# Kernel optimization log

Hardware: AMD Instinct MI355X
Metric: run time of the kernel (lower is better)

Reference implementation:

```python
import jax, jax.numpy as jnp
import numpy as np
from jax import lax

N_WAY, N_SUPPORT, N_QUERY = 16, 256, 512
D_IN, D_EMB = 4096, 1024
N_CLUSTERS, MAX_ITER = 5, 100


def setup_inputs() -> dict:
    key = jax.random.key(0)
    k1, k2, kw, kb = jax.random.split(key, 4)
    support = jax.random.normal(k1, (N_WAY, N_SUPPORT, D_IN), jnp.float32)
    query = jax.random.normal(k2, (N_WAY, N_QUERY, D_IN), jnp.float32)
    W = jax.random.normal(kw, (D_IN, D_EMB), jnp.float32) / np.float32(np.sqrt(D_IN))
    b = jax.random.normal(kb, (D_EMB,), jnp.float32) * 0.01
    return {"support": support, "query": query, "W": W, "b": b}


def _sqdist(x, c):
    # x [n,d], c [k,d] -> [n,k] squared euclidean distances
    return (jnp.sum(x * x, -1, keepdims=True)
            - 2.0 * (x @ c.T)
            + jnp.sum(c * c, -1))


def _kmeans(x, init):
    # x [n,d], init [k,d]; fixed-iteration Lloyd's kmeans (converged state is a
    # fixed point of the update, matching the torch early-break semantics).
    n = x.shape[0]
    ones = jnp.ones((n,), x.dtype)

    def step(c, _):
        assign = jnp.argmin(_sqdist(x, c), axis=1)              # [n]
        sums = jax.ops.segment_sum(x, assign, num_segments=N_CLUSTERS)
        cnt = jax.ops.segment_sum(ones, assign, num_segments=N_CLUSTERS)
        # empty cluster keeps its old centroid
        new_c = jnp.where(cnt[:, None] > 0,
                          sums / jnp.maximum(cnt, 1.0)[:, None], c)
        return new_c, None

    c, _ = lax.scan(step, init, None, length=MAX_ITER)
    return c


def _forward(support, query, W, b):
    # encoder: shared linear over flattened (n_way * n) rows
    s = (support.reshape(-1, D_IN) @ W + b).reshape(N_WAY, N_SUPPORT, D_EMB)
    q = (query.reshape(-1, D_IN) @ W + b).reshape(N_WAY, N_QUERY, D_EMB)

    # per-class kmeans init: random subset of that class's support embeddings
    keys = jax.random.split(jax.random.key(42), N_WAY)

    def init_fn(key, class_emb):
        idx = jax.random.permutation(key, N_SUPPORT)[:N_CLUSTERS]
        return class_emb[idx]

    inits = jax.vmap(init_fn)(keys, s)                 # [n_way, k, d]
    cluster_protos = jax.vmap(_kmeans)(s, inits)       # [n_way, k, d]
    class_protos = cluster_protos.mean(axis=1)         # [n_way, d]

    # cdist(query_emb [b,n,d], protos [c,d]) -> [b,n,c]
    d2 = (jnp.sum(q * q, -1)[..., None]
          - 2.0 * jnp.einsum('bnd,cd->bnc', q, class_protos)
          + jnp.sum(class_protos * class_protos, -1))
    distances = jnp.sqrt(jnp.maximum(d2, 0.0))
    return -distances                                  # logits [n_way, n_query, n_classes]


def reference(support, query, W, b):
    return _forward(support, query, W, b)
```

## Files before the change

kernel.cpp:

```cpp
#include <hip/hip_runtime.h>
#include <cstdint>
#include <cstddef>


typedef __attribute__((ext_vector_type(4))) float f32x4;
typedef __attribute__((ext_vector_type(8))) short s16x8;
typedef __attribute__((ext_vector_type(4))) short s16x4;
typedef __attribute__((ext_vector_type(8))) __bf16 bf16x8;

__device__ __forceinline__ unsigned short f2bf(float f) {
  unsigned u = __float_as_uint(f);
  return (unsigned short)((u + 0x7FFFu + ((u >> 16) & 1u)) >> 16);
}
__device__ __forceinline__ float bf2f(unsigned short h) {
  return __uint_as_float(((unsigned)h) << 16);
}

typedef const __attribute__((address_space(1))) void GV;
typedef __attribute__((address_space(3))) void LV;
__device__ __forceinline__ void gload_lds16(const void* g, void* l) {
  __builtin_amdgcn_global_load_lds((GV*)g, (LV*)l, 16, 0, 0);
}
__device__ __forceinline__ f32x4 mfma16(bf16x8 a, bf16x8 b, f32x4 c) {
  return __builtin_amdgcn_mfma_f32_16x16x32_bf16(a, b, c, 0, 0, 0);
}
__device__ __forceinline__ float wave_sum(float v) {
#pragma unroll
  for (int st = 1; st < 64; st <<= 1) v += __shfl_xor(v, st);
  return v;
}

__device__ __forceinline__ void tf2x32(unsigned k0, unsigned k1, unsigned x0,
                                       unsigned x1, unsigned& y0, unsigned& y1) {
  unsigned ks0 = k0, ks1 = k1, ks2 = k0 ^ k1 ^ 0x1BD11BDAu;
  x0 += ks0; x1 += ks1;
  const int rA[4] = {13, 15, 26, 6};
  const int rB[4] = {17, 29, 16, 24};
#define ROTL(v, d) (((v) << (d)) | ((v) >> (32 - (d))))
#define RG(R)                                     \
  _Pragma("unroll") for (int i = 0; i < 4; i++) { \
    x0 += x1; x1 = ROTL(x1, R[i]); x1 ^= x0;      \
  }
  RG(rA); x0 += ks1; x1 += ks2 + 1u;
  RG(rB); x0 += ks2; x1 += ks0 + 2u;
  RG(rA); x0 += ks0; x1 += ks1 + 3u;
  RG(rB); x0 += ks1; x1 += ks2 + 4u;
  RG(rA); x0 += ks2; x1 += ks0 + 5u;
#undef RG
#undef ROTL
  y0 = x0; y1 = x1;
}

__global__ __launch_bounds__(256) void prep_k(
    const float* __restrict__ W, const float* __restrict__ sup,
    const float* __restrict__ qry, short* __restrict__ WhiT,
    short* __restrict__ WloT, short* __restrict__ Shi,
    short* __restrict__ Slo, short* __restrict__ Qhi) {
  __shared__ float tile[64][65];
  int t = threadIdx.x;
  if (blockIdx.x < 1024) {
    int bk = blockIdx.x & 63, bn = blockIdx.x >> 6;
#pragma unroll
    for (int i = 0; i < 4; i++) {
      int row = i * 16 + (t >> 4);
      int col = (t & 15) * 4;
      f32x4 v =
          *(const f32x4*)(W + (size_t)(bk * 64 + row) * 1024 + bn * 64 + col);
      tile[row][col + 0] = v[0]; tile[row][col + 1] = v[1];
      tile[row][col + 2] = v[2]; tile[row][col + 3] = v[3];
    }
    __syncthreads();
#pragma unroll
    for (int i = 0; i < 4; i++) {
      int nrow = i * 16 + (t >> 4);
      int kcol = (t & 15) * 4;
      s16x4 hv, lv;
#pragma unroll
      for (int e = 0; e < 4; e++) {
        float v = tile[kcol + e][nrow];
        unsigned short h = f2bf(v);
        hv[e] = (short)h;
        lv[e] = (short)f2bf(v - bf2f(h));
      }
      size_t off = (size_t)(bn * 64 + nrow) * 4096 + bk * 64 + kcol;
      *(s16x4*)(WhiT + off) = hv;
      *(s16x4*)(WloT + off) = lv;
    }
  } else {
    const size_t sup_n8 = (size_t)4096 * 4096 / 8;
    const size_t tot_n8 = sup_n8 + (size_t)8192 * 4096 / 8;
    size_t stride = (size_t)(gridDim.x - 1024) * 256;
    for (size_t gid = (size_t)(blockIdx.x - 1024) * 256 + t; gid < tot_n8;
         gid += stride) {
      if (gid < sup_n8) {
        const float* src = sup + gid * 8;
        f32x4 v0 = *(const f32x4*)src, v1 = *(const f32x4*)(src + 4);
        s16x8 h, l;
#pragma unroll
        for (int e = 0; e < 4; e++) {
          unsigned short hh = f2bf(v0[e]);
          h[e] = (short)hh; l[e] = (short)f2bf(v0[e] - bf2f(hh));
        }
#pragma unroll
        for (int e = 0; e < 4; e++) {
          unsigned short hh = f2bf(v1[e]);
          h[4 + e] = (short)hh; l[4 + e] = (short)f2bf(v1[e] - bf2f(hh));
        }
        *(s16x8*)(Shi + gid * 8) = h;
        *(s16x8*)(Slo + gid * 8) = l;
      } else {
        size_t q = gid - sup_n8;
        const float* src = qry + q * 8;
        f32x4 v0 = *(const f32x4*)src, v1 = *(const f32x4*)(src + 4);
        s16x8 h;
#pragma unroll
        for (int e = 0; e < 4; e++) h[e] = (short)f2bf(v0[e]);
#pragma unroll
        for (int e = 0; e < 4; e++) h[4 + e] = (short)f2bf(v1[e]);
        *(s16x8*)(Qhi + q * 8) = h;
      }
    }
  }
}

__global__ __launch_bounds__(256) void gemm_sup_k(
    const short* __restrict__ Shi, const short* __restrict__ Slo,
    const short* __restrict__ WhiT, const short* __restrict__ WloT,
    const float* __restrict__ bias, float* __restrict__ emb) {
  __shared__ short lds[24576];
  short* Ah = lds;
  short* Al = lds + 4096;
  short* Bh = lds + 8192;
  short* Bl = lds + 16384;
  const int bid = blockIdx.x;
  const int bm = bid & 63, bn = bid >> 6;
  const int t = threadIdx.x, lane = t & 63, w = t >> 6;
  const int wr = w >> 1, wc = w & 1;
  const int fr = lane & 15, kg = lane >> 4;
  const int ls = lane >> 3, lc = lane & 7;
  const short* Ag = Shi + (size_t)bm * 64 * 4096;
  const short* Alg = Slo + (size_t)bm * 64 * 4096;
  f32x4 acc[2][4] = {};

  for (int kt = 0; kt < 64; ++kt) {
    const int k0 = kt * 64;
    __syncthreads();
    const int cch = (lc ^ ls) * 8;
#pragma unroll
    for (int j = 0; j < 2; j++) {
      int rowl = w * 16 + j * 8 + ls;
      size_t aoff = (size_t)rowl * 4096 + k0 + cch;
      int ldst = (w * 16 + j * 8) * 64;
      gload_lds16(Ag + aoff, Ah + ldst);
      gload_lds16(Alg + aoff, Al + ldst);
    }
#pragma unroll
    for (int j = 0; j < 4; j++) {
      int rowl = w * 32 + j * 8 + ls;
      size_t boff = (size_t)(bn * 128 + rowl) * 4096 + k0 + cch;
      int ldst = (w * 32 + j * 8) * 64;
      gload_lds16(WhiT + boff, Bh + ldst);
      gload_lds16(WloT + boff, Bl + ldst);
    }
    __syncthreads();
#pragma unroll
    for (int ks = 0; ks < 2; ++ks) {
      const int cx = ((ks * 4 + kg) ^ (fr & 7)) * 8;
      bf16x8 ahf[2], alf[2], bhf[4], blf[4];
#pragma unroll
      for (int mi = 0; mi < 2; mi++) {
        int arow = wr * 32 + mi * 16 + fr;
        ahf[mi] = __builtin_bit_cast(bf16x8, *(const s16x8*)(Ah + arow * 64 + cx));
        alf[mi] = __builtin_bit_cast(bf16x8, *(const s16x8*)(Al + arow * 64 + cx));
      }
#pragma unroll
      for (int ni = 0; ni < 4; ni++) {
        int brow = wc * 64 + ni * 16 + fr;
        bhf[ni] = __builtin_bit_cast(bf16x8, *(const s16x8*)(Bh + brow * 64 + cx));
        blf[ni] = __builtin_bit_cast(bf16x8, *(const s16x8*)(Bl + brow * 64 + cx));
      }
#pragma unroll
      for (int mi = 0; mi < 2; mi++)
#pragma unroll
        for (int ni = 0; ni < 4; ni++) {
          acc[mi][ni] = mfma16(ahf[mi], bhf[ni], acc[mi][ni]);
          acc[mi][ni] = mfma16(ahf[mi], blf[ni], acc[mi][ni]);
          acc[mi][ni] = mfma16(alf[mi], bhf[ni], acc[mi][ni]);
        }
    }
  }
#pragma unroll
  for (int ni = 0; ni < 4; ni++) {
    int gc = bn * 128 + wc * 64 + ni * 16 + fr;
    float bv = bias[gc];
#pragma unroll
    for (int mi = 0; mi < 2; mi++) {
      int gr = bm * 64 + wr * 32 + mi * 16 + kg * 4;
#pragma unroll
      for (int r = 0; r < 4; r++)
        emb[(size_t)(gr + r) * 1024 + gc] = acc[mi][ni][r] + bv;
    }
  }
}

__global__ __launch_bounds__(256) void gemm_qry_k(
    const short* __restrict__ Qhi, const short* __restrict__ WhiT,
    const float* __restrict__ bias, float* __restrict__ emb) {
  __shared__ short lds[16384];
  short* Ah = lds;
  short* Bh = lds + 8192;
  const int bid = blockIdx.x;
  const int bm = bid & 63, bn = bid >> 6;
  const int t = threadIdx.x, lane = t & 63, w = t >> 6;
  const int wr = w >> 1, wc = w & 1;
  const int fr = lane & 15, kg = lane >> 4;
  const int ls = lane >> 3, lc = lane & 7;
  const short* Ag = Qhi + (size_t)bm * 128 * 4096;
  f32x4 acc[4][4] = {};

  for (int kt = 0; kt < 64; ++kt) {
    const int k0 = kt * 64;
    __syncthreads();
    const int cch = (lc ^ ls) * 8;
#pragma unroll
    for (int j = 0; j < 4; j++) {
      int rowl = w * 32 + j * 8 + ls;
      size_t aoff = (size_t)rowl * 4096 + k0 + cch;
      size_t boff = (size_t)(bn * 128 + rowl) * 4096 + k0 + cch;
      int ldst = (w * 32 + j * 8) * 64;
      gload_lds16(Ag + aoff, Ah + ldst);
      gload_lds16(WhiT + boff, Bh + ldst);
    }
    __syncthreads();
#pragma unroll
    for (int ks = 0; ks < 2; ++ks) {
      const int cx = ((ks * 4 + kg) ^ (fr & 7)) * 8;
      bf16x8 ahf[4], bhf[4];
#pragma unroll
      for (int mi = 0; mi < 4; mi++) {
        int arow = wr * 64 + mi * 16 + fr;
        ahf[mi] = __builtin_bit_cast(bf16x8, *(const s16x8*)(Ah + arow * 64 + cx));
      }
#pragma unroll
      for (int ni = 0; ni < 4; ni++) {
        int brow = wc * 64 + ni * 16 + fr;
        bhf[ni] = __builtin_bit_cast(bf16x8, *(const s16x8*)(Bh + brow * 64 + cx));
      }
#pragma unroll
      for (int mi = 0; mi < 4; mi++)
#pragma unroll
        for (int ni = 0; ni < 4; ni++)
          acc[mi][ni] = mfma16(ahf[mi], bhf[ni], acc[mi][ni]);
    }
  }
#pragma unroll
  for (int ni = 0; ni < 4; ni++) {
    int gc = bn * 128 + wc * 64 + ni * 16 + fr;
    float bv = bias[gc];
#pragma unroll
    for (int mi = 0; mi < 4; mi++) {
      int gr = 4096 + bm * 128 + wr * 64 + mi * 16 + kg * 4;
#pragma unroll
      for (int r = 0; r < 4; r++)
        emb[(size_t)(gr + r) * 1024 + gc] = acc[mi][ni][r] + bv;
    }
  }
}

__global__ __launch_bounds__(256) void gemm_all_k(
    const float* __restrict__ sup, const float* __restrict__ qry,
    const short* __restrict__ WhiT, const short* __restrict__ WloT,
    const float* __restrict__ bias, float* __restrict__ emb) {
  __shared__ short lds[4 * 128 * 64];
  short* Ah = lds;
  short* Al = lds + 8192;
  short* Bh = lds + 16384;
  short* Bl = lds + 24576;
  const int bid = blockIdx.x;
  const int bm = bid % 96, bn = bid / 96;
  const bool is_sup = bm < 32;
  const int t = threadIdx.x, lane = t & 63, w = t >> 6;
  const int wr = w >> 1, wc = w & 1;
  const int fr = lane & 15, kg = lane >> 4;
  const float* Abase = is_sup ? (sup + (size_t)bm * 128 * 4096)
                              : (qry + (size_t)(bm - 32) * 128 * 4096);
  f32x4 acc[4][4] = {};
  const int ls = lane >> 3, lc = lane & 7;

  for (int kt = 0; kt < 64; ++kt) {
    const int k0 = kt * 64;
    __syncthreads();
#pragma unroll
    for (int i = 0; i < 4; i++) {
      int row = i * 32 + w * 8 + ls;
      const float* src = Abase + (size_t)row * 4096 + k0 + lc * 8;
      f32x4 v0 = *(const f32x4*)src;
      f32x4 v1 = *(const f32x4*)(src + 4);
      s16x8 hs;
#pragma unroll
      for (int e = 0; e < 4; e++) hs[e] = (short)f2bf(v0[e]);
#pragma unroll
      for (int e = 0; e < 4; e++) hs[4 + e] = (short)f2bf(v1[e]);
      int chunk = lc ^ (row & 7);
      *(s16x8*)(Ah + row * 64 + chunk * 8) = hs;
      if (is_sup) {
        s16x8 lsv;
#pragma unroll
        for (int e = 0; e < 4; e++)
          lsv[e] = (short)f2bf(v0[e] - bf2f((unsigned short)hs[e]));
#pragma unroll
        for (int e = 0; e < 4; e++)
          lsv[4 + e] = (short)f2bf(v1[e] - bf2f((unsigned short)hs[4 + e]));
        *(s16x8*)(Al + row * 64 + chunk * 8) = lsv;
      }
    }
#pragma unroll
    for (int j = 0; j < 4; j++) {
      int rowl = w * 32 + j * 8 + ls;
      int cch = (lc ^ (ls & 7)) * 8;
      size_t goff = (size_t)(bn * 128 + rowl) * 4096 + k0 + cch;
      gload_lds16(WhiT + goff, Bh + (w * 32 + j * 8) * 64);
      if (is_sup) gload_lds16(WloT + goff, Bl + (w * 32 + j * 8) * 64);
    }
    __syncthreads();
#pragma unroll
    for (int ks = 0; ks < 2; ++ks) {
      const int cx = ((ks * 4 + kg) ^ (fr & 7)) * 8;
      bf16x8 ahf[4], bhf[4];
#pragma unroll
      for (int mi = 0; mi < 4; mi++) {
        int arow = wr * 64 + mi * 16 + fr;
        ahf[mi] = __builtin_bit_cast(bf16x8, *(const s16x8*)(Ah + arow * 64 + cx));
      }
#pragma unroll
      for (int ni = 0; ni < 4; ni++) {
        int brow = wc * 64 + ni * 16 + fr;
        bhf[ni] = __builtin_bit_cast(bf16x8, *(const s16x8*)(Bh + brow * 64 + cx));
      }
      if (is_sup) {
        bf16x8 alf[4], blf[4];
#pragma unroll
        for (int mi = 0; mi < 4; mi++) {
          int arow = wr * 64 + mi * 16 + fr;
          alf[mi] =
              __builtin_bit_cast(bf16x8, *(const s16x8*)(Al + arow * 64 + cx));
        }
#pragma unroll
        for (int ni = 0; ni < 4; ni++) {
          int brow = wc * 64 + ni * 16 + fr;
          blf[ni] =
              __builtin_bit_cast(bf16x8, *(const s16x8*)(Bl + brow * 64 + cx));
        }
#pragma unroll
        for (int mi = 0; mi < 4; mi++)
#pragma unroll
          for (int ni = 0; ni < 4; ni++) {
            acc[mi][ni] = mfma16(ahf[mi], bhf[ni], acc[mi][ni]);
            acc[mi][ni] = mfma16(ahf[mi], blf[ni], acc[mi][ni]);
            acc[mi][ni] = mfma16(alf[mi], bhf[ni], acc[mi][ni]);
          }
      } else {
#pragma unroll
        for (int mi = 0; mi < 4; mi++)
#pragma unroll
          for (int ni = 0; ni < 4; ni++)
            acc[mi][ni] = mfma16(ahf[mi], bhf[ni], acc[mi][ni]);
      }
    }
  }
#pragma unroll
  for (int ni = 0; ni < 4; ni++) {
    int gc = bn * 128 + wc * 64 + ni * 16 + fr;
    float bv = bias[gc];
#pragma unroll
    for (int mi = 0; mi < 4; mi++) {
      int gr = bm * 128 + wr * 64 + mi * 16 + kg * 4;
#pragma unroll
      for (int r = 0; r < 4; r++)
        emb[(size_t)(gr + r) * 1024 + gc] = acc[mi][ni][r] + bv;
    }
  }
}

__global__ __launch_bounds__(256) void gramdiag_k(const float* __restrict__ emb,
                                                  float* __restrict__ G) {
  if (blockIdx.x < 256) {
    int c = blockIdx.x >> 4, tl = blockIdx.x & 15, ti = tl >> 2, tj = tl & 3;
    __shared__ float As[64][36];
    __shared__ float Bs[32][68];
    int t = threadIdx.x, ty = t >> 4, tx = t & 15;
    const float* base = emb + (size_t)c * 256 * 1024;
    float acc[4][4] = {};
    for (int k0 = 0; k0 < 1024; k0 += 32) {
      __syncthreads();
      {
        int r = t >> 2, seg = t & 3;
        const float* pa = base + (size_t)(ti * 64 + r) * 1024 + k0 + seg * 8;
        f32x4 va0 = *(const f32x4*)pa, va1 = *(const f32x4*)(pa + 4);
        *(f32x4*)(&As[r][seg * 8]) = va0;
        *(f32x4*)(&As[r][seg * 8 + 4]) = va1;
        const float* pb = base + (size_t)(tj * 64 + r) * 1024 + k0 + seg * 8;
        f32x4 vb0 = *(const f32x4*)pb, vb1 = *(const f32x4*)(pb + 4);
#pragma unroll
        for (int e = 0; e < 4; e++) Bs[seg * 8 + e][r] = vb0[e];
#pragma unroll
        for (int e = 0; e < 4; e++) Bs[seg * 8 + 4 + e][r] = vb1[e];
      }
      __syncthreads();
#pragma unroll 4
      for (int kk = 0; kk < 32; kk++) {
        float a0 = As[ty * 4 + 0][kk], a1 = As[ty * 4 + 1][kk];
        float a2 = As[ty * 4 + 2][kk], a3 = As[ty * 4 + 3][kk];
        f32x4 bv = *(const f32x4*)(&Bs[kk][tx * 4]);
#pragma unroll
        for (int jdx = 0; jdx < 4; jdx++) {
          acc[0][jdx] = fmaf(a0, bv[jdx], acc[0][jdx]);
          acc[1][jdx] = fmaf(a1, bv[jdx], acc[1][jdx]);
          acc[2][jdx] = fmaf(a2, bv[jdx], acc[2][jdx]);
          acc[3][jdx] = fmaf(a3, bv[jdx], acc[3][jdx]);
        }
      }
    }
#pragma unroll
    for (int i = 0; i < 4; i++) {
      int gr = ti * 64 + ty * 4 + i;
#pragma unroll
      for (int j = 0; j < 4; j++) {
        int gcl = tj * 64 + tx * 4 + j;
        if (gr != gcl)
          G[(size_t)c * 65536 + (size_t)gr * 256 + gcl] = acc[i][j];
      }
    }
  } else {
    int r = (blockIdx.x - 256) * 4 + (threadIdx.x >> 6);
    int lane = threadIdx.x & 63;
    const float* x = emb + (size_t)r * 1024;
    double acc = 0.0;
#pragma unroll
    for (int ch = 0; ch < 16; ch++) {
      float v = x[ch * 64 + lane];
      acc = fma((double)v, (double)v, acc);
    }
#pragma unroll
    for (int st = 1; st < 64; st <<= 1) acc += __shfl_xor(acc, st);
    if (lane == 0) {
      int c = r >> 8, i = r & 255;
      G[(size_t)c * 65536 + (size_t)i * 256 + i] = (float)acc;
    }
  }
}

#define APPLY1(db, nb, gg, p)                        \
  if ((db) & 1u)  s[p][0] += ((nb) & 1u)  ? (gg) : -(gg); \
  if ((db) & 2u)  s[p][1] += ((nb) & 2u)  ? (gg) : -(gg); \
  if ((db) & 4u)  s[p][2] += ((nb) & 4u)  ? (gg) : -(gg); \
  if ((db) & 8u)  s[p][3] += ((nb) & 8u)  ? (gg) : -(gg); \
  if ((db) & 16u) s[p][4] += ((nb) & 16u) ? (gg) : -(gg);

__global__ __launch_bounds__(64) void kmeans3_k(const float* __restrict__ G,
                                                float* __restrict__ wts) {
  const int c = blockIdx.x;
  const int lane = threadIdx.x;
  unsigned o0, o1, s0k, s1k;
  tf2x32(0u, 42u, 0u, (unsigned)c, o0, o1);
  tf2x32(o0, o1, 0u, 1u, s0k, s1k);
  unsigned long long key[4];
#pragma unroll
  for (int q = 0; q < 4; q++) {
    unsigned y0, y1;
    tf2x32(s0k, s1k, 0u, (unsigned)(lane + 64 * q), y0, y1);
    key[q] = ((unsigned long long)(y0 ^ y1) << 32) | (unsigned)(lane + 64 * q);
  }
  int idx5[5];
#pragma unroll
  for (int r = 0; r < 5; r++) {
    unsigned long long mn = key[0];
#pragma unroll
    for (int q = 1; q < 4; q++) mn = key[q] < mn ? key[q] : mn;
#pragma unroll
    for (int st = 1; st < 64; st <<= 1) {
      unsigned long long o = __shfl_xor(mn, st);
      mn = o < mn ? o : mn;
    }
    int widx = (int)(unsigned)(mn & 0xffffffffu);
    idx5[r] = widx;
#pragma unroll
    for (int q = 0; q < 4; q++)
      if (widx == lane + 64 * q) key[q] = ~0ull;
  }
  unsigned m[4];
#pragma unroll
  for (int q = 0; q < 4; q++) {
    unsigned mm = 0;
#pragma unroll
    for (int k = 0; k < 5; k++)
      if (idx5[k] == lane + 64 * q) mm |= 1u << k;
    m[q] = mm;
  }
  const float* Gc = G + (size_t)c * 65536;
  float s[4][5];
#pragma unroll
  for (int k = 0; k < 5; k++) {
    const float* row = Gc + (size_t)idx5[k] * 256;
#pragma unroll
    for (int q = 0; q < 4; q++) s[q][k] = row[lane + 64 * q];
  }
  float Minv[5] = {1.0f, 1.0f, 1.0f, 1.0f, 1.0f};

  for (int it = 0; it < 100; ++it) {
    float Tu[5], C2[5];
#pragma unroll
    for (int k = 0; k < 5; k++) {
      float v = 0.0f;
#pragma unroll
      for (int q = 0; q < 4; q++)
        v += ((m[q] >> k) & 1u) ? s[q][k] : 0.0f;
#pragma unroll
      for (int st = 1; st < 64; st <<= 1) v += __shfl_xor(v, st);
      float iv = Minv[k];
      Tu[k] = v * iv * iv;
      C2[k] = -2.0f * iv;
    }
    int a[4];
#pragma unroll
    for (int q = 0; q < 4; q++) {
      float d0 = fmaf(C2[0], s[q][0], Tu[0]);
      float d1 = fmaf(C2[1], s[q][1], Tu[1]);
      float d2 = fmaf(C2[2], s[q][2], Tu[2]);
      float d3 = fmaf(C2[3], s[q][3], Tu[3]);
      float d4 = fmaf(C2[4], s[q][4], Tu[4]);
      int at = 0;
      float dmn = d0;
      if (d1 < dmn) { dmn = d1; at = 1; }
      if (d2 < dmn) { dmn = d2; at = 2; }
      if (d3 < dmn) { dmn = d3; at = 3; }
      if (d4 < dmn) { dmn = d4; at = 4; }
      a[q] = at;
    }
    int cnt[5];
#pragma unroll
    for (int k = 0; k < 5; k++) {
      int v = (a[0] == k) + (a[1] == k) + (a[2] == k) + (a[3] == k);
#pragma unroll
      for (int st = 1; st < 64; st <<= 1) v += __shfl_xor(v, st);
      cnt[k] = v;
    }
    unsigned nm[4], dm[4];
#pragma unroll
    for (int q = 0; q < 4; q++) {
      unsigned nv = 0;
#pragma unroll
      for (int k = 0; k < 5; k++) {
        int bit = (cnt[k] > 0) ? (a[q] == k ? 1 : 0) : (int)((m[q] >> k) & 1u);
        nv |= ((unsigned)bit) << k;
      }
      nm[q] = nv;
      dm[q] = nv ^ m[q];
    }
    unsigned long long bal[4];
#pragma unroll
    for (int q = 0; q < 4; q++) bal[q] = __ballot(dm[q] != 0);
    if ((bal[0] | bal[1] | bal[2] | bal[3]) == 0) break;
#pragma unroll
    for (int q = 0; q < 4; q++) m[q] = nm[q];
#pragma unroll
    for (int k = 0; k < 5; k++)
      if (cnt[k] > 0) Minv[k] = 1.0f / (float)cnt[k];
#pragma unroll
    for (int q = 0; q < 4; q++) {
      unsigned long long mask = bal[q];
      while (mask) {
#define GATHER(i)                                                      \
        int j##i = -1;                                                 \
        unsigned d##i = 0, e##i = 0;                                   \
        float g##i##0 = 0, g##i##1 = 0, g##i##2 = 0, g##i##3 = 0;      \
        if (mask) {                                                    \
          j##i = __builtin_ctzll(mask);                                \
          mask &= mask - 1;                                            \
          d##i = __shfl(dm[q], j##i);                                  \
          e##i = __shfl(nm[q], j##i);                                  \
          const float* row = Gc + (size_t)(q * 64 + j##i) * 256 + lane;\
          g##i##0 = row[0];  g##i##1 = row[64];                        \
          g##i##2 = row[128]; g##i##3 = row[192];                      \
        }
        GATHER(0) GATHER(1) GATHER(2) GATHER(3)
        GATHER(4) GATHER(5) GATHER(6) GATHER(7)
#undef GATHER
#define DOAPPLY(i)                        \
        if (j##i >= 0) {                  \
          APPLY1(d##i, e##i, g##i##0, 0)  \
          APPLY1(d##i, e##i, g##i##1, 1)  \
          APPLY1(d##i, e##i, g##i##2, 2)  \
          APPLY1(d##i, e##i, g##i##3, 3)  \
        }
        DOAPPLY(0) DOAPPLY(1) DOAPPLY(2) DOAPPLY(3)
        DOAPPLY(4) DOAPPLY(5) DOAPPLY(6) DOAPPLY(7)
#undef DOAPPLY
      }
    }
  }
#pragma unroll
  for (int q = 0; q < 4; q++) {
    float wv = 0.0f;
#pragma unroll
    for (int k = 0; k < 5; k++)
      if ((m[q] >> k) & 1u) wv += 0.2f * Minv[k];
    wts[c * 256 + lane + 64 * q] = wv;
  }
}

__global__ __launch_bounds__(256) void proto1_k(const float* __restrict__ emb,
                                                const float* __restrict__ wts,
                                                float* __restrict__ part) {
  int c = blockIdx.x & 15, seg = blockIdx.x >> 4, t = threadIdx.x;
  __shared__ float wl[16];
  if (t < 16) wl[t] = wts[c * 256 + seg * 16 + t];
  __syncthreads();
  f32x4 acc = {};
  const float* base = emb + (size_t)(c * 256 + seg * 16) * 1024 + t * 4;
#pragma unroll
  for (int j = 0; j < 16; j++) {
    f32x4 v = *(const f32x4*)(base + (size_t)j * 1024);
    float wj = wl[j];
#pragma unroll
    for (int e = 0; e < 4; e++) acc[e] = fmaf(wj, v[e], acc[e]);
  }
  *(f32x4*)(part + ((size_t)seg * 16 + c) * 1024 + t * 4) = acc;
}

__global__ __launch_bounds__(256) void proto2_k(const float* __restrict__ part,
                                                float* __restrict__ protos) {
  int c = blockIdx.x, t = threadIdx.x;
  f32x4 acc = {};
#pragma unroll
  for (int seg = 0; seg < 16; seg++) {
    f32x4 v = *(const f32x4*)(part + ((size_t)seg * 16 + c) * 1024 + t * 4);
#pragma unroll
    for (int e = 0; e < 4; e++) acc[e] += v[e];
  }
  *(f32x4*)(protos + (size_t)c * 1024 + t * 4) = acc;
}

__global__ __launch_bounds__(256) void proto_k(const float* __restrict__ emb,
                                               const float* __restrict__ wts,
                                               float* __restrict__ protos) {
  int c = blockIdx.x, t = threadIdx.x;
  __shared__ float wl[256];
  wl[t] = wts[c * 256 + t];
  __syncthreads();
  f32x4 acc = {};
  const float* base = emb + (size_t)c * 256 * 1024 + t * 4;
  for (int j = 0; j < 256; j++) {
    f32x4 v = *(const f32x4*)(base + (size_t)j * 1024);
    float wj = wl[j];
#pragma unroll
    for (int e = 0; e < 4; e++) acc[e] = fmaf(wj, v[e], acc[e]);
  }
  *(f32x4*)(protos + (size_t)c * 1024 + t * 4) = acc;
}

__global__ __launch_bounds__(256) void dist_k(const float* __restrict__ emb,
                                              const float* __restrict__ protos,
                                              float* __restrict__ out) {
  __shared__ float P[16 * 1024];
  int t = threadIdx.x, lane = t & 63, w = t >> 6;
#pragma unroll
  for (int i = 0; i < 16; i++) {
    int off = i * 1024 + t * 4;
    *(f32x4*)(P + off) = *(const f32x4*)(protos + off);
  }
  __syncthreads();
  float psq_keep = 0.0f;
  for (int p = 0; p < 16; p++) {
    float partial = 0.0f;
#pragma unroll
    for (int ch = 0; ch < 16; ch++) {
      float x = P[p * 1024 + ch * 64 + lane];
      partial = fmaf(x, x, partial);
    }
    partial = wave_sum(partial);
    if (lane == p) psq_keep = partial;
  }
  const float* qbase = emb + (size_t)4096 * 1024;
  int r0 = blockIdx.x * 16 + w * 4;
  for (int ri = 0; ri < 4; ri++) {
    int row = r0 + ri;
    const float* q = qbase + (size_t)row * 1024;
    float qv[16];
#pragma unroll
    for (int ch = 0; ch < 16; ch++) qv[ch] = q[ch * 64 + lane];
    float qsq = 0.0f;
#pragma unroll
    for (int ch = 0; ch < 16; ch++) qsq = fmaf(qv[ch], qv[ch], qsq);
    qsq = wave_sum(qsq);
    float dsel = 0.0f;
    for (int p = 0; p < 16; p++) {
      float dp = 0.0f;
#pragma unroll
      for (int ch = 0; ch < 16; ch++)
        dp = fmaf(qv[ch], P[p * 1024 + ch * 64 + lane], dp);
      dp = wave_sum(dp);
      if (lane == p) dsel = dp;
    }
    if (lane < 16) {
      float d2 = qsq - 2.0f * dsel + psq_keep;
      d2 = fmaxf(d2, 0.0f);
      out[(size_t)row * 16 + lane] = -sqrtf(d2);
    }
  }
}

extern "C" void kernel_launch(void* const* d_in, const int* in_sizes, int n_in,
                              void* d_out, int out_size, void* d_ws,
                              size_t ws_size, hipStream_t stream) {
  const float* sup = (const float*)d_in[0];
  const float* qry = (const float*)d_in[1];
  const float* W = (const float*)d_in[2];
  const float* b = (const float*)d_in[3];
  float* out = (float*)d_out;
  char* ws = (char*)d_ws;
  (void)in_sizes; (void)n_in; (void)out_size;

  const size_t NEED_FAST = 206651392ULL;
  if (ws_size >= NEED_FAST) {
    short* WhiT = (short*)(ws + 0);
    short* WloT = (short*)(ws + 8388608);
    short* Shi = (short*)(ws + 16777216);
    short* Slo = (short*)(ws + 50331648);
    short* Qhi = (short*)(ws + 83886080);
    float* emb = (float*)(ws + 150994944);
    float* G = (float*)(ws + 201326592);
    float* wts = (float*)(ws + 205520896);
    float* protos = (float*)(ws + 205537280);
    float* part = (float*)(ws + 205602816);

    prep_k<<<3072, 256, 0, stream>>>(W, sup, qry, WhiT, WloT, Shi, Slo, Qhi);
    gemm_sup_k<<<512, 256, 0, stream>>>(Shi, Slo, WhiT, WloT, b, emb);
    gemm_qry_k<<<512, 256, 0, stream>>>(Qhi, WhiT, b, emb);
    gramdiag_k<<<1280, 256, 0, stream>>>(emb, G);
    kmeans3_k<<<16, 64, 0, stream>>>(G, wts);
    proto1_k<<<256, 256, 0, stream>>>(emb, wts, part);
    proto2_k<<<16, 256, 0, stream>>>(part, protos);
    dist_k<<<512, 256, 0, stream>>>(emb, protos, out);
  } else {
    short* WhiT = (short*)(ws + 0);
    short* WloT = (short*)(ws + 8388608);
    float* emb = (float*)(ws + 16777216);
    float* G = (float*)(ws + 67108864);
    float* wts = (float*)(ws + 71303168);
    float* protos = (float*)(ws + 71319552);

    prep_k<<<1024, 256, 0, stream>>>(W, sup, qry, WhiT, WloT, (short*)0,
                                     (short*)0, (short*)0);
    gemm_all_k<<<768, 256, 0, stream>>>(sup, qry, WhiT, WloT, b, emb);
    gramdiag_k<<<1280, 256, 0, stream>>>(emb, G);
    kmeans3_k<<<16, 64, 0, stream>>>(G, wts);
    proto_k<<<16, 256, 0, stream>>>(emb, wts, protos);
    dist_k<<<512, 256, 0, stream>>>(emb, protos, out);
  }
}
```

Before: 452.5 us.

## Overlap query conversion with support GEMM and Gram with query GEMM

Splits the prep kernel so the query fp32→bf16 conversion runs as extra blocks inside the support GEMM launch, and the Gram/diagonal computation on support embeddings runs as extra blocks inside the query GEMM launch. Independent work now shares a launch with a GEMM instead of running as separate serial kernels, filling idle CUs and removing launch gaps. The extra blocks compete with GEMM blocks for bandwidth and CUs. The Gram blocks depend only on support embeddings written by the previous launch.

```diff
diff --git a/kernel.cpp b/kernel.cpp
--- a/kernel.cpp
+++ b/kernel.cpp
@@ -51,11 +51,10 @@
   y0 = x0; y1 = x1;
 }
 
-__global__ __launch_bounds__(256) void prep_k(
+__global__ __launch_bounds__(256) void prep_sw_k(
     const float* __restrict__ W, const float* __restrict__ sup,
-    const float* __restrict__ qry, short* __restrict__ WhiT,
-    short* __restrict__ WloT, short* __restrict__ Shi,
-    short* __restrict__ Slo, short* __restrict__ Qhi) {
+    short* __restrict__ WhiT, short* __restrict__ WloT,
+    short* __restrict__ Shi, short* __restrict__ Slo) {
   __shared__ float tile[64][65];
   int t = threadIdx.x;
   if (blockIdx.x < 1024) {
@@ -88,181 +87,260 @@
     }
   } else {
     const size_t sup_n8 = (size_t)4096 * 4096 / 8;
-    const size_t tot_n8 = sup_n8 + (size_t)8192 * 4096 / 8;
     size_t stride = (size_t)(gridDim.x - 1024) * 256;
-    for (size_t gid = (size_t)(blockIdx.x - 1024) * 256 + t; gid < tot_n8;
+    for (size_t gid = (size_t)(blockIdx.x - 1024) * 256 + t; gid < sup_n8;
          gid += stride) {
-      if (gid < sup_n8) {
-        const float* src = sup + gid * 8;
-        f32x4 v0 = *(const f32x4*)src, v1 = *(const f32x4*)(src + 4);
-        s16x8 h, l;
-#pragma unroll
-        for (int e = 0; e < 4; e++) {
-          unsigned short hh = f2bf(v0[e]);
-          h[e] = (short)hh; l[e] = (short)f2bf(v0[e] - bf2f(hh));
-        }
-#pragma unroll
-        for (int e = 0; e < 4; e++) {
-          unsigned short hh = f2bf(v1[e]);
-          h[4 + e] = (short)hh; l[4 + e] = (short)f2bf(v1[e] - bf2f(hh));
-        }
-        *(s16x8*)(Shi + gid * 8) = h;
-        *(s16x8*)(Slo + gid * 8) = l;
-      } else {
-        size_t q = gid - sup_n8;
-        const float* src = qry + q * 8;
-        f32x4 v0 = *(const f32x4*)src, v1 = *(const f32x4*)(src + 4);
-        s16x8 h;
-#pragma unroll
-        for (int e = 0; e < 4; e++) h[e] = (short)f2bf(v0[e]);
-#pragma unroll
-        for (int e = 0; e < 4; e++) h[4 + e] = (short)f2bf(v1[e]);
-        *(s16x8*)(Qhi + q * 8) = h;
-      }
-    }
-  }
-}
-
-__global__ __launch_bounds__(256) void gemm_sup_k(
+      const float* src = sup + gid * 8;
+      f32x4 v0 = *(const f32x4*)src, v1 = *(const f32x4*)(src + 4);
+      s16x8 h, l;
+#pragma unroll
+      for (int e = 0; e < 4; e++) {
+        unsigned short hh = f2bf(v0[e]);
+        h[e] = (short)hh; l[e] = (short)f2bf(v0[e] - bf2f(hh));
+      }
+#pragma unroll
+      for (int e = 0; e < 4; e++) {
+        unsigned short hh = f2bf(v1[e]);
+        h[4 + e] = (short)hh; l[4 + e] = (short)f2bf(v1[e] - bf2f(hh));
+      }
+      *(s16x8*)(Shi + gid * 8) = h;
+      *(s16x8*)(Slo + gid * 8) = l;
+    }
+  }
+}
+
+__global__ __launch_bounds__(256) void gemm_supq_k(
     const short* __restrict__ Shi, const short* __restrict__ Slo,
     const short* __restrict__ WhiT, const short* __restrict__ WloT,
-    const float* __restrict__ bias, float* __restrict__ emb) {
+    const float* __restrict__ bias, float* __restrict__ emb,
+    const float* __restrict__ qry, short* __restrict__ Qhi) {
   __shared__ short lds[24576];
-  short* Ah = lds;
-  short* Al = lds + 4096;
-  short* Bh = lds + 8192;
-  short* Bl = lds + 16384;
-  const int bid = blockIdx.x;
-  const int bm = bid & 63, bn = bid >> 6;
-  const int t = threadIdx.x, lane = t & 63, w = t >> 6;
-  const int wr = w >> 1, wc = w & 1;
-  const int fr = lane & 15, kg = lane >> 4;
-  const int ls = lane >> 3, lc = lane & 7;
-  const short* Ag = Shi + (size_t)bm * 64 * 4096;
-  const short* Alg = Slo + (size_t)bm * 64 * 4096;
-  f32x4 acc[2][4] = {};
-
-  for (int kt = 0; kt < 64; ++kt) {
-    const int k0 = kt * 64;
-    __syncthreads();
-    const int cch = (lc ^ ls) * 8;
-#pragma unroll
-    for (int j = 0; j < 2; j++) {
-      int rowl = w * 16 + j * 8 + ls;
-      size_t aoff = (size_t)rowl * 4096 + k0 + cch;
-      int ldst = (w * 16 + j * 8) * 64;
-      gload_lds16(Ag + aoff, Ah + ldst);
-      gload_lds16(Alg + aoff, Al + ldst);
-    }
-#pragma unroll
-    for (int j = 0; j < 4; j++) {
-      int rowl = w * 32 + j * 8 + ls;
-      size_t boff = (size_t)(bn * 128 + rowl) * 4096 + k0 + cch;
-      int ldst = (w * 32 + j * 8) * 64;
-      gload_lds16(WhiT + boff, Bh + ldst);
-      gload_lds16(WloT + boff, Bl + ldst);
-    }
-    __syncthreads();
-#pragma unroll
-    for (int ks = 0; ks < 2; ++ks) {
-      const int cx = ((ks * 4 + kg) ^ (fr & 7)) * 8;
-      bf16x8 ahf[2], alf[2], bhf[4], blf[4];
+  const int t = threadIdx.x;
+  if (blockIdx.x < 512) {
+    short* Ah = lds;
+    short* Al = lds + 4096;
+    short* Bh = lds + 8192;
+    short* Bl = lds + 16384;
+    const int bid = blockIdx.x;
+    const int bm = bid & 63, bn = bid >> 6;
+    const int lane = t & 63, w = t >> 6;
+    const int wr = w >> 1, wc = w & 1;
+    const int fr = lane & 15, kg = lane >> 4;
+    const int ls = lane >> 3, lc = lane & 7;
+    const short* Ag = Shi + (size_t)bm * 64 * 4096;
+    const short* Alg = Slo + (size_t)bm * 64 * 4096;
+    f32x4 acc[2][4] = {};
+
+    for (int kt = 0; kt < 64; ++kt) {
+      const int k0 = kt * 64;
+      __syncthreads();
+      const int cch = (lc ^ ls) * 8;
+#pragma unroll
+      for (int j = 0; j < 2; j++) {
+        int rowl = w * 16 + j * 8 + ls;
+        size_t aoff = (size_t)rowl * 4096 + k0 + cch;
+        int ldst = (w * 16 + j * 8) * 64;
+        gload_lds16(Ag + aoff, Ah + ldst);
+        gload_lds16(Alg + aoff, Al + ldst);
+      }
+#pragma unroll
+      for (int j = 0; j < 4; j++) {
+        int rowl = w * 32 + j * 8 + ls;
+        size_t boff = (size_t)(bn * 128 + rowl) * 4096 + k0 + cch;
+        int ldst = (w * 32 + j * 8) * 64;
+        gload_lds16(WhiT + boff, Bh + ldst);
+        gload_lds16(WloT + boff, Bl + ldst);
+      }
+      __syncthreads();
+#pragma unroll
+      for (int ks = 0; ks < 2; ++ks) {
+        const int cx = ((ks * 4 + kg) ^ (fr & 7)) * 8;
+        bf16x8 ahf[2], alf[2], bhf[4], blf[4];
+#pragma unroll
+        for (int mi = 0; mi < 2; mi++) {
+          int arow = wr * 32 + mi * 16 + fr;
+          ahf[mi] =
+              __builtin_bit_cast(bf16x8, *(const s16x8*)(Ah + arow * 64 + cx));
+          alf[mi] =
+              __builtin_bit_cast(bf16x8, *(const s16x8*)(Al + arow * 64 + cx));
+        }
+#pragma unroll
+        for (int ni = 0; ni < 4; ni++) {
+          int brow = wc * 64 + ni * 16 + fr;
+          bhf[ni] =
+              __builtin_bit_cast(bf16x8, *(const s16x8*)(Bh + brow * 64 + cx));
+          blf[ni] =
+              __builtin_bit_cast(bf16x8, *(const s16x8*)(Bl + brow * 64 + cx));
+        }
+#pragma unroll
+        for (int mi = 0; mi < 2; mi++)
+#pragma unroll
+          for (int ni = 0; ni < 4; ni++) {
+            acc[mi][ni] = mfma16(ahf[mi], bhf[ni], acc[mi][ni]);
+            acc[mi][ni] = mfma16(ahf[mi], blf[ni], acc[mi][ni]);
+            acc[mi][ni] = mfma16(alf[mi], bhf[ni], acc[mi][ni]);
+          }
+      }
+    }
+#pragma unroll
+    for (int ni = 0; ni < 4; ni++) {
+      int gc = bn * 128 + wc * 64 + ni * 16 + fr;
+      float bv = bias[gc];
 #pragma unroll
       for (int mi = 0; mi < 2; mi++) {
-        int arow = wr * 32 + mi * 16 + fr;
-        ahf[mi] = __builtin_bit_cast(bf16x8, *(const s16x8*)(Ah + arow * 64 + cx));
-        alf[mi] = __builtin_bit_cast(bf16x8, *(const s16x8*)(Al + arow * 64 + cx));
-      }
-#pragma unroll
-      for (int ni = 0; ni < 4; ni++) {
-        int brow = wc * 64 + ni * 16 + fr;
-        bhf[ni] = __builtin_bit_cast(bf16x8, *(const s16x8*)(Bh + brow * 64 + cx));
-        blf[ni] = __builtin_bit_cast(bf16x8, *(const s16x8*)(Bl + brow * 64 + cx));
-      }
-#pragma unroll
-      for (int mi = 0; mi < 2; mi++)
+        int gr = bm * 64 + wr * 32 + mi * 16 + kg * 4;
+#pragma unroll
+        for (int r = 0; r < 4; r++)
+          emb[(size_t)(gr + r) * 1024 + gc] = acc[mi][ni][r] + bv;
+      }
+    }
+  } else {
+    const size_t qry_n8 = (size_t)8192 * 4096 / 8;
+    size_t stride = (size_t)(gridDim.x - 512) * 256;
+    for (size_t gid = (size_t)(blockIdx.x - 512) * 256 + t; gid < qry_n8;
+         gid += stride) {
+      const float* src = qry + gid * 8;
+      f32x4 v0 = *(const f32x4*)src, v1 = *(const f32x4*)(src + 4);
+      s16x8 h;
+#pragma unroll
+      for (int e = 0; e < 4; e++) h[e] = (short)f2bf(v0[e]);
+#pragma unroll
+      for (int e = 0; e < 4; e++) h[4 + e] = (short)f2bf(v1[e]);
+      *(s16x8*)(Qhi + gid * 8) = h;
+    }
+  }
+}
+
+__global__ __launch_bounds__(256) void gemm_qry_gram_k(
+    const short* __restrict__ Qhi, const short* __restrict__ WhiT,
+    const float* __restrict__ bias, float* __restrict__ emb,
+    float* __restrict__ G) {
+  __shared__ __align__(16) char smem[32768];
+  const int t = threadIdx.x;
+  if (blockIdx.x < 512) {
+    short* Ah = (short*)smem;
+    short* Bh = (short*)(smem + 16384);
+    const int bid = blockIdx.x;
+    const int bm = bid & 63, bn = bid >> 6;
+    const int lane = t & 63, w = t >> 6;
+    const int wr = w >> 1, wc = w & 1;
+    const int fr = lane & 15, kg = lane >> 4;
+    const int ls = lane >> 3, lc = lane & 7;
+    const short* Ag = Qhi + (size_t)bm * 128 * 4096;
+    f32x4 acc[4][4] = {};
+
+    for (int kt = 0; kt < 64; ++kt) {
+      const int k0 = kt * 64;
+      __syncthreads();
+      const int cch = (lc ^ ls) * 8;
+#pragma unroll
+      for (int j = 0; j < 4; j++) {
+        int rowl = w * 32 + j * 8 + ls;
+        size_t aoff = (size_t)rowl * 4096 + k0 + cch;
+        size_t boff = (size_t)(bn * 128 + rowl) * 4096 + k0 + cch;
+        int ldst = (w * 32 + j * 8) * 64;
+        gload_lds16(Ag + aoff, Ah + ldst);
+        gload_lds16(WhiT + boff, Bh + ldst);
+      }
+      __syncthreads();
+#pragma unroll
+      for (int ks = 0; ks < 2; ++ks) {
+        const int cx = ((ks * 4 + kg) ^ (fr & 7)) * 8;
+        bf16x8 ahf[4], bhf[4];
+#pragma unroll
+        for (int mi = 0; mi < 4; mi++) {
+          int arow = wr * 64 + mi * 16 + fr;
+          ahf[mi] =
+              __builtin_bit_cast(bf16x8, *(const s16x8*)(Ah + arow * 64 + cx));
+        }
 #pragma unroll
         for (int ni = 0; ni < 4; ni++) {
-          acc[mi][ni] = mfma16(ahf[mi], bhf[ni], acc[mi][ni]);
-          acc[mi][ni] = mfma16(ahf[mi], blf[ni], acc[mi][ni]);
-          acc[mi][ni] = mfma16(alf[mi], bhf[ni], acc[mi][ni]);
-        }
-    }
-  }
-#pragma unroll
-  for (int ni = 0; ni < 4; ni++) {
-    int gc = bn * 128 + wc * 64 + ni * 16 + fr;
-    float bv = bias[gc];
-#pragma unroll
-    for (int mi = 0; mi < 2; mi++) {
-      int gr = bm * 64 + wr * 32 + mi * 16 + kg * 4;
-#pragma unroll
-      for (int r = 0; r < 4; r++)
-        emb[(size_t)(gr + r) * 1024 + gc] = acc[mi][ni][r] + bv;
-    }
-  }
-}
-
-__global__ __launch_bounds__(256) void gemm_qry_k(
-    const short* __restrict__ Qhi, const short* __restrict__ WhiT,
-    const float* __restrict__ bias, float* __restrict__ emb) {
-  __shared__ short lds[16384];
-  short* Ah = lds;
-  short* Bh = lds + 8192;
-  const int bid = blockIdx.x;
-  const int bm = bid & 63, bn = bid >> 6;
-  const int t = threadIdx.x, lane = t & 63, w = t >> 6;
-  const int wr = w >> 1, wc = w & 1;
-  const int fr = lane & 15, kg = lane >> 4;
-  const int ls = lane >> 3, lc = lane & 7;
-  const short* Ag = Qhi + (size_t)bm * 128 * 4096;
-  f32x4 acc[4][4] = {};
-
-  for (int kt = 0; kt < 64; ++kt) {
-    const int k0 = kt * 64;
-    __syncthreads();
-    const int cch = (lc ^ ls) * 8;
-#pragma unroll
-    for (int j = 0; j < 4; j++) {
-      int rowl = w * 32 + j * 8 + ls;
-      size_t aoff = (size_t)rowl * 4096 + k0 + cch;
-      size_t boff = (size_t)(bn * 128 + rowl) * 4096 + k0 + cch;
-      int ldst = (w * 32 + j * 8) * 64;
-      gload_lds16(Ag + aoff, Ah + ldst);
-      gload_lds16(WhiT + boff, Bh + ldst);
-    }
-    __syncthreads();
-#pragma unroll
-    for (int ks = 0; ks < 2; ++ks) {
-      const int cx = ((ks * 4 + kg) ^ (fr & 7)) * 8;
-      bf16x8 ahf[4], bhf[4];
+          int brow = wc * 64 + ni * 16 + fr;
+          bhf[ni] =
+              __builtin_bit_cast(bf16x8, *(const s16x8*)(Bh + brow * 64 + cx));
+        }
+#pragma unroll
+        for (int mi = 0; mi < 4; mi++)
+#pragma unroll
+          for (int ni = 0; ni < 4; ni++)
+            acc[mi][ni] = mfma16(ahf[mi], bhf[ni], acc[mi][ni]);
+      }
+    }
+#pragma unroll
+    for (int ni = 0; ni < 4; ni++) {
+      int gc = bn * 128 + wc * 64 + ni * 16 + fr;
+      float bv = bias[gc];
 #pragma unroll
       for (int mi = 0; mi < 4; mi++) {
-        int arow = wr * 64 + mi * 16 + fr;
-        ahf[mi] = __builtin_bit_cast(bf16x8, *(const s16x8*)(Ah + arow * 64 + cx));
-      }
-#pragma unroll
-      for (int ni = 0; ni < 4; ni++) {
-        int brow = wc * 64 + ni * 16 + fr;
-        bhf[ni] = __builtin_bit_cast(bf16x8, *(const s16x8*)(Bh + brow * 64 + cx));
-      }
-#pragma unroll
-      for (int mi = 0; mi < 4; mi++)
-#pragma unroll
-        for (int ni = 0; ni < 4; ni++)
-          acc[mi][ni] = mfma16(ahf[mi], bhf[ni], acc[mi][ni]);
-    }
-  }
-#pragma unroll
-  for (int ni = 0; ni < 4; ni++) {
-    int gc = bn * 128 + wc * 64 + ni * 16 + fr;
-    float bv = bias[gc];
-#pragma unroll
-    for (int mi = 0; mi < 4; mi++) {
-      int gr = 4096 + bm * 128 + wr * 64 + mi * 16 + kg * 4;
-#pragma unroll
-      for (int r = 0; r < 4; r++)
-        emb[(size_t)(gr + r) * 1024 + gc] = acc[mi][ni][r] + bv;
+        int gr = 4096 + bm * 128 + wr * 64 + mi * 16 + kg * 4;
+#pragma unroll
+        for (int r = 0; r < 4; r++)
+          emb[(size_t)(gr + r) * 1024 + gc] = acc[mi][ni][r] + bv;
+      }
+    }
+  } else if (blockIdx.x < 768) {
+    int bb = blockIdx.x - 512;
+    int c = bb >> 4, tl = bb & 15, ti = tl >> 2, tj = tl & 3;
+    float (*As)[36] = (float(*)[36])smem;
+    float (*Bs)[68] = (float(*)[68])(smem + 9216);
+    int ty = t >> 4, tx = t & 15;
+    const float* base = emb + (size_t)c * 256 * 1024;
+    float acc[4][4] = {};
+    for (int k0 = 0; k0 < 1024; k0 += 32) {
+      __syncthreads();
+      {
+        int r = t >> 2, seg = t & 3;
+        const float* pa = base + (size_t)(ti * 64 + r) * 1024 + k0 + seg * 8;
+        f32x4 va0 = *(const f32x4*)pa, va1 = *(const f32x4*)(pa + 4);
+        *(f32x4*)(&As[r][seg * 8]) = va0;
+        *(f32x4*)(&As[r][seg * 8 + 4]) = va1;
+        const float* pb = base + (size_t)(tj * 64 + r) * 1024 + k0 + seg * 8;
+        f32x4 vb0 = *(const f32x4*)pb, vb1 = *(const f32x4*)(pb + 4);
+#pragma unroll
+        for (int e = 0; e < 4; e++) Bs[seg * 8 + e][r] = vb0[e];
+#pragma unroll
+        for (int e = 0; e < 4; e++) Bs[seg * 8 + 4 + e][r] = vb1[e];
+      }
+      __syncthreads();
+#pragma unroll 4
+      for (int kk = 0; kk < 32; kk++) {
+        float a0 = As[ty * 4 + 0][kk], a1 = As[ty * 4 + 1][kk];
+        float a2 = As[ty * 4 + 2][kk], a3 = As[ty * 4 + 3][kk];
+        f32x4 bv = *(const f32x4*)(&Bs[kk][tx * 4]);
+#pragma unroll
+        for (int jdx = 0; jdx < 4; jdx++) {
+          acc[0][jdx] = fmaf(a0, bv[jdx], acc[0][jdx]);
+          acc[1][jdx] = fmaf(a1, bv[jdx], acc[1][jdx]);
+          acc[2][jdx] = fmaf(a2, bv[jdx], acc[2][jdx]);
+          acc[3][jdx] = fmaf(a3, bv[jdx], acc[3][jdx]);
+        }
+      }
+    }
+#pragma unroll
+    for (int i = 0; i < 4; i++) {
+      int gr = ti * 64 + ty * 4 + i;
+#pragma unroll
+      for (int j = 0; j < 4; j++) {
+        int gcl = tj * 64 + tx * 4 + j;
+        if (gr != gcl)
+          G[(size_t)c * 65536 + (size_t)gr * 256 + gcl] = acc[i][j];
+      }
+    }
+  } else {
+    int r = (blockIdx.x - 768) * 4 + (t >> 6);
+    int lane = t & 63;
+    const float* x = emb + (size_t)r * 1024;
+    double acc = 0.0;
+#pragma unroll
+    for (int ch = 0; ch < 16; ch++) {
+      float v = x[ch * 64 + lane];
+      acc = fma((double)v, (double)v, acc);
+    }
+#pragma unroll
+    for (int st = 1; st < 64; st <<= 1) acc += __shfl_xor(acc, st);
+    if (lane == 0) {
+      int c = r >> 8, i = r & 255;
+      G[(size_t)c * 65536 + (size_t)i * 256 + i] = (float)acc;
     }
   }
 }
@@ -734,10 +812,10 @@
     float* protos = (float*)(ws + 205537280);
     float* part = (float*)(ws + 205602816);
 
-    prep_k<<<3072, 256, 0, stream>>>(W, sup, qry, WhiT, WloT, Shi, Slo, Qhi);
-    gemm_sup_k<<<512, 256, 0, stream>>>(Shi, Slo, WhiT, WloT, b, emb);
-    gemm_qry_k<<<512, 256, 0, stream>>>(Qhi, WhiT, b, emb);
-    gramdiag_k<<<1280, 256, 0, stream>>>(emb, G);
+    prep_sw_k<<<2048, 256, 0, stream>>>(W, sup, WhiT, WloT, Shi, Slo);
+    gemm_supq_k<<<768, 256, 0, stream>>>(Shi, Slo, WhiT, WloT, b, emb, qry,
+                                         Qhi);
+    gemm_qry_gram_k<<<1792, 256, 0, stream>>>(Qhi, WhiT, b, emb, G);
     kmeans3_k<<<16, 64, 0, stream>>>(G, wts);
     proto1_k<<<256, 256, 0, stream>>>(emb, wts, part);
     proto2_k<<<16, 256, 0, stream>>>(part, protos);
@@ -750,8 +828,8 @@
     float* wts = (float*)(ws + 71303168);
     float* protos = (float*)(ws + 71319552);
 
-    prep_k<<<1024, 256, 0, stream>>>(W, sup, qry, WhiT, WloT, (short*)0,
-                                     (short*)0, (short*)0);
+    prep_sw_k<<<1024, 256, 0, stream>>>(W, sup, WhiT, WloT, (short*)0,
+                                        (short*)0);
     gemm_all_k<<<768, 256, 0, stream>>>(sup, qry, WhiT, WloT, b, emb);
     gramdiag_k<<<1280, 256, 0, stream>>>(emb, G);
     kmeans3_k<<<16, 64, 0, stream>>>(G, wts);
```

After: 440.3 us. 2.7% less time.
